# Performance work log

Hardware: AMD Instinct MI355X
Metric: run time of the kernel (lower is better)

The kernel has to match this reference:

```python
import jax, jax.numpy as jnp
import numpy as np

B, S, HID = 1, 2048, 2048
NH, NKV = 32, 8
HD = HID // NH  # 64
WINDOW = 1024
ROPE_BASE = 500000.0


def setup_inputs() -> dict:
    key = jax.random.key(0)
    ks = jax.random.split(key, 5)
    sc = 0.02
    return {
        "hidden_states": jax.random.normal(ks[0], (B, S, HID), dtype=jnp.float32),
        "Wq": jax.random.normal(ks[1], (HID, NH * HD), dtype=jnp.float32) * sc,
        "Wk": jax.random.normal(ks[2], (HID, NKV * HD), dtype=jnp.float32) * sc,
        "Wv": jax.random.normal(ks[3], (HID, NKV * HD), dtype=jnp.float32) * sc,
        "Wo": jax.random.normal(ks[4], (NH * HD, HID), dtype=jnp.float32) * sc,
    }


def _rope_cos_sin(seq_len, dtype):
    inv_freq = 1.0 / (ROPE_BASE ** (jnp.arange(0, HD, 2, dtype=jnp.float32) / HD))
    pos = jnp.arange(seq_len, dtype=jnp.float32)
    freqs = pos[:, None] * inv_freq[None, :]          # [S, HD/2]
    emb = jnp.concatenate([freqs, freqs], axis=-1)    # [S, HD]
    return jnp.cos(emb).astype(dtype), jnp.sin(emb).astype(dtype)


def _rotate_half(x):
    x1, x2 = x[..., : HD // 2], x[..., HD // 2:]
    return jnp.concatenate([-x2, x1], axis=-1)


def reference(hidden_states, Wq, Wk, Wv, Wo):
    b, s, _ = hidden_states.shape
    q = (hidden_states @ Wq).reshape(b, s, NH, HD).transpose(0, 2, 1, 3)   # [B,NH,S,D]
    k = (hidden_states @ Wk).reshape(b, s, NKV, HD).transpose(0, 2, 1, 3)  # [B,NKV,S,D]
    v = (hidden_states @ Wv).reshape(b, s, NKV, HD).transpose(0, 2, 1, 3)

    cos, sin = _rope_cos_sin(s, hidden_states.dtype)  # [S, D]
    cos, sin = cos[None, None], sin[None, None]       # [1,1,S,D]
    q = q * cos + _rotate_half(q) * sin
    k = k * cos + _rotate_half(k) * sin

    n_rep = NH // NKV
    k = jnp.repeat(k, n_rep, axis=1)  # [B,NH,S,D]
    v = jnp.repeat(v, n_rep, axis=1)

    # sliding-window causal additive mask
    row = jnp.arange(s)[:, None]
    col = jnp.arange(s)[None, :]
    banned = (col > row) | (col < row - WINDOW + 1)
    mask = jnp.where(banned, jnp.float32(-jnp.inf), 0.0).astype(hidden_states.dtype)

    scale = 1.0 / np.sqrt(HD)
    scores = jnp.einsum("bhqd,bhkd->bhqk", q, k) * scale + mask
    attn = jax.nn.softmax(scores, axis=-1)
    out = jnp.einsum("bhqk,bhkd->bhqd", attn, v)          # [B,NH,S,D]
    out = out.transpose(0, 2, 1, 3).reshape(b, s, NH * HD)
    return out @ Wo
```

## Files before the change

### kernel.cpp

```cpp
#include <hip/hip_runtime.h>
#include <hip/hip_bf16.h>
#include <math.h>

#define S_LEN 2048
#define HID 2048
#define NH 32
#define NKV 8
#define HD 64
#define WINDOW 1024
#define QBLK 128
#define QKVN 3072

typedef __attribute__((ext_vector_type(8))) short bx8;
typedef __attribute__((ext_vector_type(4))) float fx4;
typedef __attribute__((ext_vector_type(8))) unsigned short us8;

#define GL_LDS16(gp, lp) \
    __builtin_amdgcn_global_load_lds((__attribute__((address_space(1))) const void*)(gp), \
                                     (__attribute__((address_space(3))) void*)(lp), 16, 0, 0)

__global__ __launch_bounds__(256) void prep_kernel(const float* __restrict__ hs,
                                                   const float* __restrict__ Wq,
                                                   const float* __restrict__ Wk,
                                                   const float* __restrict__ Wv,
                                                   const float* __restrict__ Wo,
                                                   float* __restrict__ cosT, float* __restrict__ sinT,
                                                   __hip_bfloat16* __restrict__ hsb,
                                                   __hip_bfloat16* __restrict__ WqkvT,
                                                   __hip_bfloat16* __restrict__ WoT) {
    __shared__ float tile[32][33];
    int b = blockIdx.x, t = threadIdx.x;
    if (b < 256) {
        int idx = b * 256 + t;
        int s = idx >> 5, f = idx & 31;
        double inv = exp(-2.0 * (double)f / 64.0 * log(500000.0));
        double ang = (double)s * inv;
        cosT[idx] = (float)cos(ang);
        sinT[idx] = (float)sin(ang);
        return;
    }
    b -= 256;
    if (b < 2048) {
        int i = (b * 256 + t) * 8;
        float4 a = *reinterpret_cast<const float4*>(&hs[i]);
        float4 c = *reinterpret_cast<const float4*>(&hs[i + 4]);
        __hip_bfloat16 o[8] __attribute__((aligned(16)));
        o[0] = __float2bfloat16(a.x); o[1] = __float2bfloat16(a.y);
        o[2] = __float2bfloat16(a.z); o[3] = __float2bfloat16(a.w);
        o[4] = __float2bfloat16(c.x); o[5] = __float2bfloat16(c.y);
        o[6] = __float2bfloat16(c.z); o[7] = __float2bfloat16(c.w);
        *reinterpret_cast<bx8*>(&hsb[i]) = *reinterpret_cast<bx8*>(o);
        return;
    }
    b -= 2048;
    const float* src; __hip_bfloat16* dst; int Nd, bx, by;
    if (b < 4096)      { src = Wq; dst = WqkvT;                        Nd = 2048; bx = b & 63; by = b >> 6; }
    else if (b < 5120) { b -= 4096; src = Wk; dst = WqkvT + (size_t)2048 * 2048; Nd = 512; bx = b & 15; by = b >> 4; }
    else if (b < 6144) { b -= 5120; src = Wv; dst = WqkvT + (size_t)2560 * 2048; Nd = 512; bx = b & 15; by = b >> 4; }
    else               { b -= 6144; src = Wo; dst = WoT;               Nd = 2048; bx = b & 63; by = b >> 6; }
    int n0 = bx * 32, k0 = by * 32, tx = t & 31, ty = t >> 5;
#pragma unroll
    for (int i = 0; i < 4; i++)
        tile[ty + 8 * i][tx] = src[(size_t)(k0 + ty + 8 * i) * Nd + n0 + tx];
    __syncthreads();
#pragma unroll
    for (int i = 0; i < 4; i++)
        dst[(size_t)(n0 + ty + 8 * i) * 2048 + k0 + tx] = __float2bfloat16(tile[tx][ty + 8 * i]);
}

__global__ __launch_bounds__(256) void ropev_kernel(__hip_bfloat16* __restrict__ QKV,
                                                    __hip_bfloat16* __restrict__ Vt,
                                                    const float* __restrict__ cosT,
                                                    const float* __restrict__ sinT) {
    __shared__ __hip_bfloat16 tile[32][33];
    int b = blockIdx.x, t = threadIdx.x;
    if (b < 10240) {
        int idx = b * 256 + t;
        int f = idx & 31;
        int head = (idx >> 5) % (NH + NKV);
        int s = idx / ((NH + NKV) * 32);
        float c  = cosT[(s << 5) + f];
        float sn = sinT[(s << 5) + f];
        __hip_bfloat16* p = (head < NH) ? (QKV + (size_t)s * QKVN + head * HD)
                                        : (QKV + (size_t)s * QKVN + 2048 + (head - NH) * HD);
        float x1 = __bfloat162float(p[f]), x2 = __bfloat162float(p[f + 32]);
        p[f]      = __float2bfloat16(x1 * c - x2 * sn);
        p[f + 32] = __float2bfloat16(x2 * c + x1 * sn);
        return;
    }
    b -= 10240;
    int s0 = (b & 63) * 32, d0 = (b >> 6) * 32;
    int tx = t & 31, ty = t >> 5;
#pragma unroll
    for (int i = 0; i < 4; i++)
        tile[ty + 8 * i][tx] = QKV[(size_t)(s0 + ty + 8 * i) * QKVN + 2560 + d0 + tx];
    __syncthreads();
#pragma unroll
    for (int i = 0; i < 4; i++)
        Vt[(size_t)(d0 + ty + 8 * i) * S_LEN + s0 + tx] = tile[tx][ty + 8 * i];
}

template <int OUTBF16>
__global__ __launch_bounds__(256) void gemm_pipe_kernel(const __hip_bfloat16* __restrict__ A,
                                                        const __hip_bfloat16* __restrict__ Bt,
                                                        void* __restrict__ Cp,
                                                        int M, int N, int K, int stripe) {
    __shared__ __hip_bfloat16 As[3][2048];
    __shared__ __hip_bfloat16 Bs[3][4096];

    const int bid = blockIdx.x;
    const int x = bid & 7, j = bid >> 3;
    const int bn = (x * stripe + j % stripe) * 128;
    const int bm = (j / stripe) * 64;

    const int t = threadIdx.x, w = t >> 6, l = t & 63;
    const int wr = (w >> 1) * 32, wc = (w & 1) * 64;
    const int lr = l & 15;
    const int rdslot = (((l >> 4) ^ ((lr >> 1) & 3))) * 8;
    const int srow = w * 16 + (l >> 2);
    const int scol = (((l & 3) ^ ((l >> 3) & 3))) * 8;
    const int ldsoff = w * 512;

    const __hip_bfloat16* ga0 = A + (size_t)(bm + srow) * K + scol;
    const __hip_bfloat16* gb0 = Bt + (size_t)(bn + srow) * K + scol;
    const size_t half = (size_t)64 * K;

    fx4 acc[2][4];
#pragma unroll
    for (int m = 0; m < 2; m++)
#pragma unroll
        for (int n = 0; n < 4; n++) acc[m][n] = (fx4){0.f, 0.f, 0.f, 0.f};

    const int T = K >> 5;

#define STAGE(kt, b)                                              \
    do {                                                          \
        const __hip_bfloat16* ga = ga0 + (kt) * 32;               \
        const __hip_bfloat16* gb = gb0 + (kt) * 32;               \
        GL_LDS16(ga,        &As[(b)][ldsoff]);                    \
        GL_LDS16(gb,        &Bs[(b)][ldsoff]);                    \
        GL_LDS16(gb + half, &Bs[(b)][2048 + ldsoff]);             \
    } while (0)

    STAGE(0, 0);
    STAGE(1, 1);

    for (int i = 0; i < T; i++) {
        const int r = i % 3;
        if (i + 1 < T) asm volatile("s_waitcnt vmcnt(3)" ::: "memory");
        else           asm volatile("s_waitcnt vmcnt(0)" ::: "memory");
        __builtin_amdgcn_s_barrier();
        asm volatile("" ::: "memory");
        if (i + 2 < T) STAGE(i + 2, (i + 2) % 3);

        bx8 af[2], bf[4];
#pragma unroll
        for (int m = 0; m < 2; m++)
            af[m] = *reinterpret_cast<const bx8*>(&As[r][(wr + m * 16 + lr) * 32 + rdslot]);
#pragma unroll
        for (int n = 0; n < 4; n++)
            bf[n] = *reinterpret_cast<const bx8*>(&Bs[r][(wc + n * 16 + lr) * 32 + rdslot]);
#pragma unroll
        for (int m = 0; m < 2; m++)
#pragma unroll
            for (int n = 0; n < 4; n++)
                acc[m][n] = __builtin_amdgcn_mfma_f32_16x16x32_bf16(af[m], bf[n], acc[m][n], 0, 0, 0);
    }
#undef STAGE

    const int lq = (l >> 4) * 4;
#pragma unroll
    for (int m = 0; m < 2; m++)
#pragma unroll
        for (int n = 0; n < 4; n++)
#pragma unroll
            for (int r2 = 0; r2 < 4; r2++) {
                int row = bm + wr + m * 16 + lq + r2;
                int col = bn + wc + n * 16 + lr;
                float v = acc[m][n][r2];
                if (OUTBF16)
                    ((__hip_bfloat16*)Cp)[(size_t)row * N + col] = __float2bfloat16(v);
                else
                    ((float*)Cp)[(size_t)row * N + col] = v;
            }
}

__global__ __launch_bounds__(512, 4) void attn_kernel(const __hip_bfloat16* __restrict__ Q,
                                                      const __hip_bfloat16* __restrict__ Kg,
                                                      const __hip_bfloat16* __restrict__ Vtg,
                                                      __hip_bfloat16* __restrict__ Ab) {
    __shared__ __hip_bfloat16 Ks[2][4096];
    __shared__ __hip_bfloat16 Vs[2][4096];
    __shared__ __hip_bfloat16 Ps[QBLK * 64];

    const int bid = blockIdx.x;
    const int swz = (bid & 7) * 64 + (bid >> 3);
    const int h = swz >> 4, qi = swz & 15;
    const int qb = qi * QBLK;
    const int kvh = h >> 2;

    const int t = threadIdx.x, w = t >> 6, l = t & 63;
    const int lr = l & 15, g = l >> 4, lk = g * 8;
    const int qbw = qb + 16 * w;
    const int prow = 16 * w + lr;
    const int psz = (prow & 7) << 4;

    char* PsB = (char*)Ps;

    bx8 qa[2];
#pragma unroll
    for (int ks = 0; ks < 2; ks++)
        qa[ks] = *reinterpret_cast<const bx8*>(
            &Q[(size_t)(qbw + lr) * QKVN + h * HD + ks * 32 + lk]);

    fx4 ot[4];
#pragma unroll
    for (int n = 0; n < 4; n++) ot[n] = (fx4){0.f, 0.f, 0.f, 0.f};
    float mrow = -1e30f, srow = 0.f;

    const int k0_first = (qb >= 1024) ? (qb - 1024) : 0;
    const int k0_last  = qb + 64;
    const int wmax = qbw + 15;
    const int rowq = qbw + lr;

    const int sr = t >> 3, c8 = t & 7;
    const int scolsw = 8 * (c8 ^ (sr & 7));
    const int kcol = kvh * HD + scolsw;
    const int vrow = kvh * HD + sr;
    __hip_bfloat16* ldsK = &Ks[0][0] + (t >> 6) * 512;
    __hip_bfloat16* ldsV = &Vs[0][0] + (t >> 6) * 512;

#define ASTAGE(k0v, p)                                                           \
    do {                                                                         \
        GL_LDS16(&Kg[(size_t)((k0v) + sr) * QKVN + kcol], ldsK + (p) * 4096);    \
        GL_LDS16(&Vtg[(size_t)vrow * S_LEN + (k0v) + scolsw], ldsV + (p) * 4096);\
    } while (0)

    ASTAGE(k0_first, 0);

    int ti = 0;
    for (int k0 = k0_first; k0 <= k0_last; k0 += 64, ++ti) {
        const int p = ti & 1;
        asm volatile("s_waitcnt vmcnt(0)" ::: "memory");
        __builtin_amdgcn_s_barrier();
        asm volatile("" ::: "memory");
        if (k0 + 64 <= k0_last) ASTAGE(k0 + 64, p ^ 1);

        if (k0 <= wmax) {
            char* KsB = (char*)&Ks[p][0];
            char* VsB = (char*)&Vs[p][0];
            bx8 kb[4][2];
#pragma unroll
            for (int n = 0; n < 4; n++)
#pragma unroll
                for (int ks = 0; ks < 2; ks++) {
                    int row = 16 * n + lr;
                    kb[n][ks] = *reinterpret_cast<const bx8*>(
                        KsB + row * 128 + (((ks * 64) + 16 * g) ^ ((row & 7) << 4)));
                }
            fx4 sc[4];
#pragma unroll
            for (int n = 0; n < 4; n++) {
                sc[n] = __builtin_amdgcn_mfma_f32_16x16x32_bf16(kb[n][0], qa[0],
                                                                (fx4){0.f, 0.f, 0.f, 0.f}, 0, 0, 0);
                sc[n] = __builtin_amdgcn_mfma_f32_16x16x32_bf16(kb[n][1], qa[1], sc[n], 0, 0, 0);
            }
            const bool interior = (k0 + 63 <= qbw) && (k0 >= qbw - 1008);
            if (interior) {
#pragma unroll
                for (int n = 0; n < 4; n++)
#pragma unroll
                    for (int r = 0; r < 4; r++) sc[n][r] *= 0.125f;
            } else {
#pragma unroll
                for (int n = 0; n < 4; n++)
#pragma unroll
                    for (int r = 0; r < 4; r++) {
                        int key = k0 + 16 * n + 4 * g + r;
                        bool valid = (key <= rowq) && (key >= rowq - (WINDOW - 1));
                        sc[n][r] = valid ? sc[n][r] * 0.125f : -1e30f;
                    }
            }
            float tmax = fmaxf(fmaxf(sc[0][0], sc[0][1]), fmaxf(sc[0][2], sc[0][3]));
#pragma unroll
            for (int n = 1; n < 4; n++)
                tmax = fmaxf(tmax, fmaxf(fmaxf(sc[n][0], sc[n][1]), fmaxf(sc[n][2], sc[n][3])));
            tmax = fmaxf(tmax, __shfl_xor(tmax, 16));
            tmax = fmaxf(tmax, __shfl_xor(tmax, 32));
            float mn = fmaxf(mrow, tmax);
            float fs = __expf(mrow - mn);
            mrow = mn;
            float ps = 0.f;
#pragma unroll
            for (int n = 0; n < 4; n++) {
#pragma unroll
                for (int r = 0; r < 4; r++) {
                    float p2 = __expf(sc[n][r] - mn);
                    sc[n][r] = p2;
                    ps += p2;
                }
                __hip_bfloat16 pk[4] __attribute__((aligned(8)));
                pk[0] = __float2bfloat16(sc[n][0]); pk[1] = __float2bfloat16(sc[n][1]);
                pk[2] = __float2bfloat16(sc[n][2]); pk[3] = __float2bfloat16(sc[n][3]);
                *reinterpret_cast<unsigned long long*>(PsB + prow * 128 + ((32 * n + 8 * g) ^ psz)) =
                    *reinterpret_cast<unsigned long long*>(pk);
            }
            ps += __shfl_xor(ps, 16);
            ps += __shfl_xor(ps, 32);
            srow = srow * fs + ps;
#pragma unroll
            for (int n = 0; n < 4; n++)
#pragma unroll
                for (int r = 0; r < 4; r++) ot[n][r] *= fs;
            bx8 vb[4][2];
#pragma unroll
            for (int n = 0; n < 4; n++)
#pragma unroll
                for (int ks = 0; ks < 2; ks++) {
                    int row = 16 * n + lr;
                    vb[n][ks] = *reinterpret_cast<const bx8*>(
                        VsB + row * 128 + (((ks * 64) + 16 * g) ^ ((row & 7) << 4)));
                }
            bx8 pb[2];
#pragma unroll
            for (int ks = 0; ks < 2; ks++)
                pb[ks] = *reinterpret_cast<const bx8*>(
                    PsB + prow * 128 + (((ks * 64) + 16 * g) ^ psz));
#pragma unroll
            for (int n = 0; n < 4; n++) {
                ot[n] = __builtin_amdgcn_mfma_f32_16x16x32_bf16(vb[n][0], pb[0], ot[n], 0, 0, 0);
                ot[n] = __builtin_amdgcn_mfma_f32_16x16x32_bf16(vb[n][1], pb[1], ot[n], 0, 0, 0);
            }
        }
    }
#undef ASTAGE

    const float inv = 1.f / srow;
#pragma unroll
    for (int n = 0; n < 4; n++) {
        __hip_bfloat16 pk[4] __attribute__((aligned(8)));
#pragma unroll
        for (int r = 0; r < 4; r++) pk[r] = __float2bfloat16(ot[n][r] * inv);
        *reinterpret_cast<unsigned long long*>(PsB + prow * 128 + ((32 * n + 8 * g) ^ psz)) =
            *reinterpret_cast<unsigned long long*>(pk);
    }
    __syncthreads();
#pragma unroll
    for (int j = 0; j < 2; j++) {
        const int row = (t >> 3) + 64 * j, c = t & 7;
        us8 v = *reinterpret_cast<const us8*>(PsB + row * 128 + ((c * 16) ^ ((row & 7) << 4)));
        *reinterpret_cast<us8*>(&Ab[(size_t)(qb + row) * HID + h * HD + c * 8]) = v;
    }
}

extern "C" void kernel_launch(void* const* d_in, const int* in_sizes, int n_in,
                              void* d_out, int out_size, void* d_ws, size_t ws_size,
                              hipStream_t stream) {
    const float* hs = (const float*)d_in[0];
    const float* Wq = (const float*)d_in[1];
    const float* Wk = (const float*)d_in[2];
    const float* Wv = (const float*)d_in[3];
    const float* Wo = (const float*)d_in[4];

    float* ws   = (float*)d_ws;
    float* cosT = ws;
    float* sinT = cosT + 65536;
    __hip_bfloat16* hsb    = (__hip_bfloat16*)(sinT + 65536);
    __hip_bfloat16* WqkvT  = hsb + 4194304;
    __hip_bfloat16* WoT    = WqkvT + 6291456;
    __hip_bfloat16* QKVb   = WoT + 4194304;
    __hip_bfloat16* Vt     = QKVb + 6291456;
    __hip_bfloat16* Ab     = hsb;

    prep_kernel<<<12544, 256, 0, stream>>>(hs, Wq, Wk, Wv, Wo, cosT, sinT, hsb, WqkvT, WoT);

    gemm_pipe_kernel<1><<<768, 256, 0, stream>>>(hsb, WqkvT, QKVb, 2048, QKVN, 2048, 3);

    ropev_kernel<<<11264, 256, 0, stream>>>(QKVb, Vt, cosT, sinT);

    attn_kernel<<<512, 512, 0, stream>>>(QKVb, QKVb + 2048, Vt, Ab);

    gemm_pipe_kernel<0><<<512, 256, 0, stream>>>(Ab, WoT, d_out, 2048, 2048, 2048, 2);
}
```

Baseline: 144.7 us.

## Double attention query block to 256 rows with two M-fragments per wave

Each attention workgroup now covers 256 query rows instead of 128. Each wave handles two 16-row fragments that share the K/V tiles already loaded into LDS, so K/V global traffic and LDS fragment loads are amortized over twice the queries. The cost is half as many workgroups (256 on a large-CU device), lower occupancy (launch bounds drop from 4 to 2), more registers, and more masked work at the causal edge per block.

```diff
diff --git a/kernel.cpp b/kernel.cpp
--- a/kernel.cpp
+++ b/kernel.cpp
@@ -8,7 +8,7 @@
 #define NKV 8
 #define HD 64
 #define WINDOW 1024
-#define QBLK 128
+#define QBLK 256
 #define QKVN 3072
 
 typedef __attribute__((ext_vector_type(8))) short bx8;
@@ -185,7 +185,7 @@
             }
 }
 
-__global__ __launch_bounds__(512, 4) void attn_kernel(const __hip_bfloat16* __restrict__ Q,
+__global__ __launch_bounds__(512, 2) void attn_kernel(const __hip_bfloat16* __restrict__ Q,
                                                       const __hip_bfloat16* __restrict__ Kg,
                                                       const __hip_bfloat16* __restrict__ Vtg,
                                                       __hip_bfloat16* __restrict__ Ab) {
@@ -194,34 +194,37 @@
     __shared__ __hip_bfloat16 Ps[QBLK * 64];
 
     const int bid = blockIdx.x;
-    const int swz = (bid & 7) * 64 + (bid >> 3);
-    const int h = swz >> 4, qi = swz & 15;
+    const int swz = (bid & 7) * 32 + (bid >> 3);
+    const int h = swz >> 3, qi = swz & 7;
     const int qb = qi * QBLK;
     const int kvh = h >> 2;
 
     const int t = threadIdx.x, w = t >> 6, l = t & 63;
     const int lr = l & 15, g = l >> 4, lk = g * 8;
-    const int qbw = qb + 16 * w;
-    const int prow = 16 * w + lr;
-    const int psz = (prow & 7) << 4;
+    const int qbw = qb + 32 * w;
 
     char* PsB = (char*)Ps;
 
-    bx8 qa[2];
-#pragma unroll
-    for (int ks = 0; ks < 2; ks++)
-        qa[ks] = *reinterpret_cast<const bx8*>(
-            &Q[(size_t)(qbw + lr) * QKVN + h * HD + ks * 32 + lk]);
-
-    fx4 ot[4];
-#pragma unroll
-    for (int n = 0; n < 4; n++) ot[n] = (fx4){0.f, 0.f, 0.f, 0.f};
-    float mrow = -1e30f, srow = 0.f;
+    bx8 qa[2][2];
+#pragma unroll
+    for (int mf = 0; mf < 2; mf++)
+#pragma unroll
+        for (int ks = 0; ks < 2; ks++)
+            qa[mf][ks] = *reinterpret_cast<const bx8*>(
+                &Q[(size_t)(qbw + 16 * mf + lr) * QKVN + h * HD + ks * 32 + lk]);
+
+    fx4 ot[2][4];
+    float mrow[2], srow[2];
+#pragma unroll
+    for (int mf = 0; mf < 2; mf++) {
+        mrow[mf] = -1e30f; srow[mf] = 0.f;
+#pragma unroll
+        for (int n = 0; n < 4; n++) ot[mf][n] = (fx4){0.f, 0.f, 0.f, 0.f};
+    }
 
     const int k0_first = (qb >= 1024) ? (qb - 1024) : 0;
-    const int k0_last  = qb + 64;
-    const int wmax = qbw + 15;
-    const int rowq = qbw + lr;
+    const int k0_last  = qb + 192;
+    const int wmax = qbw + 31;
 
     const int sr = t >> 3, c8 = t & 7;
     const int scolsw = 8 * (c8 ^ (sr & 7));
@@ -258,60 +261,67 @@
                     kb[n][ks] = *reinterpret_cast<const bx8*>(
                         KsB + row * 128 + (((ks * 64) + 16 * g) ^ ((row & 7) << 4)));
                 }
-            fx4 sc[4];
-#pragma unroll
-            for (int n = 0; n < 4; n++) {
-                sc[n] = __builtin_amdgcn_mfma_f32_16x16x32_bf16(kb[n][0], qa[0],
-                                                                (fx4){0.f, 0.f, 0.f, 0.f}, 0, 0, 0);
-                sc[n] = __builtin_amdgcn_mfma_f32_16x16x32_bf16(kb[n][1], qa[1], sc[n], 0, 0, 0);
+#pragma unroll
+            for (int mf = 0; mf < 2; mf++) {
+                const int rowq = qbw + 16 * mf + lr;
+                const int prow = 32 * w + 16 * mf + lr;
+                const int psz = (prow & 7) << 4;
+                fx4 sc[4];
+#pragma unroll
+                for (int n = 0; n < 4; n++) {
+                    sc[n] = __builtin_amdgcn_mfma_f32_16x16x32_bf16(kb[n][0], qa[mf][0],
+                                                                    (fx4){0.f, 0.f, 0.f, 0.f}, 0, 0, 0);
+                    sc[n] = __builtin_amdgcn_mfma_f32_16x16x32_bf16(kb[n][1], qa[mf][1], sc[n], 0, 0, 0);
+                }
+                const int qlow = qbw + 16 * mf;
+                const bool interior = (k0 + 63 <= qlow) && (k0 >= qlow - 1008);
+                if (interior) {
+#pragma unroll
+                    for (int n = 0; n < 4; n++)
+#pragma unroll
+                        for (int r = 0; r < 4; r++) sc[n][r] *= 0.125f;
+                } else {
+#pragma unroll
+                    for (int n = 0; n < 4; n++)
+#pragma unroll
+                        for (int r = 0; r < 4; r++) {
+                            int key = k0 + 16 * n + 4 * g + r;
+                            bool valid = (key <= rowq) && (key >= rowq - (WINDOW - 1));
+                            sc[n][r] = valid ? sc[n][r] * 0.125f : -1e30f;
+                        }
+                }
+                float tmax = fmaxf(fmaxf(sc[0][0], sc[0][1]), fmaxf(sc[0][2], sc[0][3]));
+#pragma unroll
+                for (int n = 1; n < 4; n++)
+                    tmax = fmaxf(tmax, fmaxf(fmaxf(sc[n][0], sc[n][1]), fmaxf(sc[n][2], sc[n][3])));
+                tmax = fmaxf(tmax, __shfl_xor(tmax, 16));
+                tmax = fmaxf(tmax, __shfl_xor(tmax, 32));
+                float mn = fmaxf(mrow[mf], tmax);
+                float fs = __expf(mrow[mf] - mn);
+                mrow[mf] = mn;
+                float ps = 0.f;
+#pragma unroll
+                for (int n = 0; n < 4; n++) {
+#pragma unroll
+                    for (int r = 0; r < 4; r++) {
+                        float p2 = __expf(sc[n][r] - mn);
+                        sc[n][r] = p2;
+                        ps += p2;
+                    }
+                    __hip_bfloat16 pk[4] __attribute__((aligned(8)));
+                    pk[0] = __float2bfloat16(sc[n][0]); pk[1] = __float2bfloat16(sc[n][1]);
+                    pk[2] = __float2bfloat16(sc[n][2]); pk[3] = __float2bfloat16(sc[n][3]);
+                    *reinterpret_cast<unsigned long long*>(PsB + prow * 128 + ((32 * n + 8 * g) ^ psz)) =
+                        *reinterpret_cast<unsigned long long*>(pk);
+                }
+                ps += __shfl_xor(ps, 16);
+                ps += __shfl_xor(ps, 32);
+                srow[mf] = srow[mf] * fs + ps;
+#pragma unroll
+                for (int n = 0; n < 4; n++)
+#pragma unroll
+                    for (int r = 0; r < 4; r++) ot[mf][n][r] *= fs;
             }
-            const bool interior = (k0 + 63 <= qbw) && (k0 >= qbw - 1008);
-            if (interior) {
-#pragma unroll
-                for (int n = 0; n < 4; n++)
-#pragma unroll
-                    for (int r = 0; r < 4; r++) sc[n][r] *= 0.125f;
-            } else {
-#pragma unroll
-                for (int n = 0; n < 4; n++)
-#pragma unroll
-                    for (int r = 0; r < 4; r++) {
-                        int key = k0 + 16 * n + 4 * g + r;
-                        bool valid = (key <= rowq) && (key >= rowq - (WINDOW - 1));
-                        sc[n][r] = valid ? sc[n][r] * 0.125f : -1e30f;
-                    }
-            }
-            float tmax = fmaxf(fmaxf(sc[0][0], sc[0][1]), fmaxf(sc[0][2], sc[0][3]));
-#pragma unroll
-            for (int n = 1; n < 4; n++)
-                tmax = fmaxf(tmax, fmaxf(fmaxf(sc[n][0], sc[n][1]), fmaxf(sc[n][2], sc[n][3])));
-            tmax = fmaxf(tmax, __shfl_xor(tmax, 16));
-            tmax = fmaxf(tmax, __shfl_xor(tmax, 32));
-            float mn = fmaxf(mrow, tmax);
-            float fs = __expf(mrow - mn);
-            mrow = mn;
-            float ps = 0.f;
-#pragma unroll
-            for (int n = 0; n < 4; n++) {
-#pragma unroll
-                for (int r = 0; r < 4; r++) {
-                    float p2 = __expf(sc[n][r] - mn);
-                    sc[n][r] = p2;
-                    ps += p2;
-                }
-                __hip_bfloat16 pk[4] __attribute__((aligned(8)));
-                pk[0] = __float2bfloat16(sc[n][0]); pk[1] = __float2bfloat16(sc[n][1]);
-                pk[2] = __float2bfloat16(sc[n][2]); pk[3] = __float2bfloat16(sc[n][3]);
-                *reinterpret_cast<unsigned long long*>(PsB + prow * 128 + ((32 * n + 8 * g) ^ psz)) =
-                    *reinterpret_cast<unsigned long long*>(pk);
-            }
-            ps += __shfl_xor(ps, 16);
-            ps += __shfl_xor(ps, 32);
-            srow = srow * fs + ps;
-#pragma unroll
-            for (int n = 0; n < 4; n++)
-#pragma unroll
-                for (int r = 0; r < 4; r++) ot[n][r] *= fs;
             bx8 vb[4][2];
 #pragma unroll
             for (int n = 0; n < 4; n++)
@@ -321,32 +331,42 @@
                     vb[n][ks] = *reinterpret_cast<const bx8*>(
                         VsB + row * 128 + (((ks * 64) + 16 * g) ^ ((row & 7) << 4)));
                 }
-            bx8 pb[2];
-#pragma unroll
-            for (int ks = 0; ks < 2; ks++)
-                pb[ks] = *reinterpret_cast<const bx8*>(
-                    PsB + prow * 128 + (((ks * 64) + 16 * g) ^ psz));
-#pragma unroll
-            for (int n = 0; n < 4; n++) {
-                ot[n] = __builtin_amdgcn_mfma_f32_16x16x32_bf16(vb[n][0], pb[0], ot[n], 0, 0, 0);
-                ot[n] = __builtin_amdgcn_mfma_f32_16x16x32_bf16(vb[n][1], pb[1], ot[n], 0, 0, 0);
+#pragma unroll
+            for (int mf = 0; mf < 2; mf++) {
+                const int prow = 32 * w + 16 * mf + lr;
+                const int psz = (prow & 7) << 4;
+                bx8 pb[2];
+#pragma unroll
+                for (int ks = 0; ks < 2; ks++)
+                    pb[ks] = *reinterpret_cast<const bx8*>(
+                        PsB + prow * 128 + (((ks * 64) + 16 * g) ^ psz));
+#pragma unroll
+                for (int n = 0; n < 4; n++) {
+                    ot[mf][n] = __builtin_amdgcn_mfma_f32_16x16x32_bf16(vb[n][0], pb[0], ot[mf][n], 0, 0, 0);
+                    ot[mf][n] = __builtin_amdgcn_mfma_f32_16x16x32_bf16(vb[n][1], pb[1], ot[mf][n], 0, 0, 0);
+                }
             }
         }
     }
 #undef ASTAGE
 
-    const float inv = 1.f / srow;
-#pragma unroll
-    for (int n = 0; n < 4; n++) {
-        __hip_bfloat16 pk[4] __attribute__((aligned(8)));
-#pragma unroll
-        for (int r = 0; r < 4; r++) pk[r] = __float2bfloat16(ot[n][r] * inv);
-        *reinterpret_cast<unsigned long long*>(PsB + prow * 128 + ((32 * n + 8 * g) ^ psz)) =
-            *reinterpret_cast<unsigned long long*>(pk);
+#pragma unroll
+    for (int mf = 0; mf < 2; mf++) {
+        const int prow = 32 * w + 16 * mf + lr;
+        const int psz = (prow & 7) << 4;
+        const float inv = 1.f / srow[mf];
+#pragma unroll
+        for (int n = 0; n < 4; n++) {
+            __hip_bfloat16 pk[4] __attribute__((aligned(8)));
+#pragma unroll
+            for (int r = 0; r < 4; r++) pk[r] = __float2bfloat16(ot[mf][n][r] * inv);
+            *reinterpret_cast<unsigned long long*>(PsB + prow * 128 + ((32 * n + 8 * g) ^ psz)) =
+                *reinterpret_cast<unsigned long long*>(pk);
+        }
     }
     __syncthreads();
 #pragma unroll
-    for (int j = 0; j < 2; j++) {
+    for (int j = 0; j < 4; j++) {
         const int row = (t >> 3) + 64 * j, c = t & 7;
         us8 v = *reinterpret_cast<const us8*>(PsB + row * 128 + ((c * 16) ^ ((row & 7) << 4)));
         *reinterpret_cast<us8*>(&Ab[(size_t)(qb + row) * HID + h * HD + c * 8]) = v;
@@ -378,7 +398,7 @@
 
     ropev_kernel<<<11264, 256, 0, stream>>>(QKVb, Vt, cosT, sinT);
 
-    attn_kernel<<<512, 512, 0, stream>>>(QKVb, QKVb + 2048, Vt, Ab);
+    attn_kernel<<<256, 512, 0, stream>>>(QKVb, QKVb + 2048, Vt, Ab);
 
     gemm_pipe_kernel<0><<<512, 256, 0, stream>>>(Ab, WoT, d_out, 2048, 2048, 2048, 2);
 }
```

Measured after the change: 153.9 us. +6.3%, slower.
